# Performance work log

Measured on AMD Instinct MI355X. Metric: run time of the kernel, lower is better.

The kernel has to match this reference:

```python
import jax, jax.numpy as jnp
import numpy as np


def setup_inputs() -> dict:
    key = jax.random.key(0)
    k1, k2 = jax.random.split(key, 2)
    B, C, N, O, K = 4, 3, 8192, 64, 20
    x = jax.random.normal(k1, (B, C, N), dtype=jnp.float32)          # point cloud [B,3,N]
    W = jax.random.normal(k2, (O, 2 * C), dtype=jnp.float32) * 0.1   # 1x1 conv weight on 2C edge features
    b = jnp.zeros((O,), dtype=jnp.float32)
    return {"x": x, "W": W, "b": b, "k": K}


def _knn_idx(x, k):
    # x: [B, C, N]. Same math as torch knn(): pd = -||xi||^2 + 2 xi.xj - ||xj||^2,
    # topk of pd (largest) == k nearest neighbors.
    inner = -2.0 * jnp.einsum('bcn,bcm->bnm', x, x)      # [B,N,N]
    xx = jnp.sum(x * x, axis=1)                          # [B,N]
    pd = -xx[:, :, None] - inner - xx[:, None, :]        # [B,N,N] negative sq-dist
    _, idx = jax.lax.top_k(pd, k)                        # [B,N,k]
    return idx


def reference(x, W, b, k):
    # Faithful jax version of knn + get_graph_feature + 1x1 conv + LeakyReLU + max over k
    # (DGCNN EdgeConv layer, the hot path of the encoder).
    B, C, N = x.shape
    idx = _knn_idx(x, k)                                  # [B,N,k]
    xt = jnp.transpose(x, (0, 2, 1))                      # [B,N,C]
    nb = xt[jnp.arange(B)[:, None, None], idx]            # gather neighbors [B,N,k,C]
    cen = xt[:, :, None, :]                               # [B,N,1,C]
    feat = jnp.concatenate(
        [nb - cen, jnp.broadcast_to(cen, (B, N, k, C))], axis=-1)  # [B,N,k,2C]
    h = jnp.einsum('bnkc,oc->bonk', feat, W) + b[None, :, None, None]  # [B,O,N,k]
    h = jax.nn.leaky_relu(h, negative_slope=0.2)
    return jnp.max(h, axis=-1)                            # [B,O,N]
```

## Files before the change

kernel.cpp:

```cpp
#include <hip/hip_runtime.h>
#include <cstdint>

#pragma clang fp contract(off)

#define N_PTS 8192
#define B_SZ  4
#define K_NN  20
#define O_CH  64
#define QW    64
#define NWAVE 8
#define WARM  64
#define CAPQ  56
#define SPADQ 57
#define NCH   5

typedef unsigned long long u64k;

__device__ __forceinline__ float pd_np(float qx, float qy, float qz, float xxn,
                                       float cx, float cy, float cz, float xm) {
  float p0 = qx * cx;
  float p1 = qy * cy;
  float p2 = qz * cz;
  float dot = (p0 + p1) + p2;
  float t = __builtin_fmaf(dot, 2.0f, -xxn);
  return t - xm;
}

__device__ __forceinline__ void insert20(float (&arr)[K_NN], float v) {
  float c = v;
#pragma unroll
  for (int u = K_NN - 1; u >= 0; --u) {
    float hi = fmaxf(arr[u], c);
    c = fminf(arr[u], c);
    arr[u] = hi;
  }
}

__device__ __forceinline__ void insK(u64k (&a)[K_NN], u64k k) {
  u64k c = k;
#pragma unroll
  for (int u = K_NN - 1; u >= 0; --u) {
    bool g = a[u] > c;
    u64k hi = g ? a[u] : c;
    u64k lo = g ? c : a[u];
    a[u] = hi;
    c = lo;
  }
}

__device__ __forceinline__ unsigned sortable32(float pd) {
  unsigned s = __float_as_uint(pd);
  return s ^ ((unsigned)((int)s >> 31) | 0x80000000u);
}

__device__ __forceinline__ u64k packKey(float pd, int j) {
  return ((u64k)sortable32(pd) << 13) | (unsigned)(8191 - j);
}

__device__ __forceinline__ float keyPd(u64k k) {
  unsigned sp = (unsigned)(k >> 13);
  unsigned s = (sp & 0x80000000u) ? (sp & 0x7FFFFFFFu) : ~sp;
  return __uint_as_float(s);
}

__global__ __launch_bounds__(256, 2)
void pack_kernel(const float* __restrict__ x, float4* __restrict__ P) {
  int idx = blockIdx.x * 256 + threadIdx.x;
  if (idx >= B_SZ * N_PTS) return;
  int b = idx >> 13;
  int n = idx & (N_PTS - 1);
  const float* xb = x + (size_t)b * 3 * N_PTS;
  float x0 = xb[n];
  float x1 = xb[n + N_PTS];
  float x2 = xb[n + 2 * N_PTS];
  float xxv = (x0 * x0 + x1 * x1) + x2 * x2;
  P[idx] = make_float4(x0, x1, x2, xxv);
}

__global__ __launch_bounds__(512, 4)
void knn_edgeconv_kernel(const float4* __restrict__ P,
                         const float* __restrict__ W,
                         const float* __restrict__ bias,
                         float* __restrict__ out) {
  __shared__ u64k  smem[5376];
  __shared__ float tau_l[QW];
  __shared__ int   cnt_l[QW];
  __shared__ int   list_l[QW][21];

  const int t  = threadIdx.x;
  const int ql = t & 63;
  const int s  = t >> 6;
  const int wb = blockIdx.x;
  const int b  = wb >> 7;
  const int n0 = (wb & 127) << 6;
  const int q  = n0 + ql;

  const float4* __restrict__ Pb = P + (size_t)b * N_PTS;
  const float4* __restrict__ Pq = Pb + n0;

  const float4 qc = Pb[q];
  const float qx = qc.x, qy = qc.y, qz = qc.z, xxn = qc.w;

  const int sw  = __builtin_amdgcn_readfirstlane(s);
  const int myq = (sw << 3) + ql;

  float arrv[K_NN];
#pragma unroll
  for (int i = 0; i < K_NN; ++i) arrv[i] = -__builtin_inff();
  {
    const int jb = sw * WARM;
    for (int jj = 0; jj < WARM; ++jj) {
      float4 cd = Pb[jb + jj];
      float pdv = pd_np(qx, qy, qz, xxn, cd.x, cd.y, cd.z, cd.w);
      if (pdv > arrv[0]) insert20(arrv, pdv);
    }
    float* WV = (float*)smem;
#pragma unroll
    for (int i = 0; i < K_NN; ++i) WV[t * 21 + i] = arrv[i];
  }
  __syncthreads();

  u64k karr[K_NN];
#pragma unroll
  for (int i = 0; i < K_NN; ++i) karr[i] = 0ULL;
  if (ql < 8) {
    const float* WV = (const float*)smem;
    float m[K_NN];
#pragma unroll
    for (int i = 0; i < K_NN; ++i) m[i] = -__builtin_inff();
    for (int p = 0; p < NWAVE; ++p) {
      const float* pv = WV + ((p << 6) + myq) * 21;
      for (int i = 0; i < K_NN; ++i) {
        float v = pv[i];
        if (v > m[0]) insert20(m, v);
      }
    }
    tau_l[myq] = m[0];
    cnt_l[myq] = 0;
  }
  __syncthreads();

  const int CB[NCH + 1] = {0, 512, 1024, 2048, 4096, 8192};
  u64k* stk = smem;

  for (int c = 0; c < NCH; ++c) {
    {
      const int csz  = CB[c + 1] - CB[c];
      const int nbat = csz >> 9;
      const int jb   = CB[c] + sw * (csz >> 3);
      const int tau_own = __float_as_int(tau_l[ql]);
      for (int bt = 0; bt < nbat; ++bt) {
        const int j = jb + (bt << 6) + ql;
        const float4 cd = Pb[j];
        const float cx = cd.x, cy = cd.y, cz = cd.z, cw = cd.w;
#pragma unroll 4
        for (int qi = 0; qi < QW; ++qi) {
          const float4 qv = Pq[qi];
          const float stau = __int_as_float(__builtin_amdgcn_readlane(tau_own, qi));
          float pdv = pd_np(qv.x, qv.y, qv.z, qv.w, cx, cy, cz, cw);
          if (pdv >= stau) {
            int slot = atomicAdd(&cnt_l[qi], 1);
            if (slot < CAPQ)
              stk[qi * SPADQ + slot] =
                  ((u64k)__float_as_uint(pdv) << 32) | (unsigned)j;
          }
        }
      }
    }
    __syncthreads();

    if (ql < 8) {
      const float tauc = tau_l[myq];
      const int pc = cnt_l[myq];
      if (pc <= CAPQ) {
        for (int i = 0; i < pc; ++i) {
          u64k e = stk[myq * SPADQ + i];
          float pdv = __uint_as_float((unsigned)(e >> 32));
          int jv = (int)(e & 0xFFFFFFFFu);
          u64k k = packKey(pdv, jv);
          if (k > karr[0]) insK(karr, k);
        }
      } else {
        float4 mq = Pq[myq];
        for (int j = CB[c]; j < CB[c + 1]; ++j) {
          float4 cd = Pb[j];
          float pdv = pd_np(mq.x, mq.y, mq.z, mq.w, cd.x, cd.y, cd.z, cd.w);
          if (pdv >= tauc) {
            u64k k = packKey(pdv, j);
            if (k > karr[0]) insK(karr, k);
          }
        }
      }
      cnt_l[myq] = 0;
      float t20 = keyPd(karr[0]);
      tau_l[myq] = fmaxf(tauc, t20);
    }
    __syncthreads();
  }

  if (ql < 8) {
#pragma unroll
    for (int i = 0; i < K_NN; ++i)
      list_l[myq][i] = 8191 - (int)(karr[i] & 8191ULL);
  }
  __syncthreads();

  float acc[8];
#pragma unroll
  for (int oi = 0; oi < 8; ++oi) acc[oi] = -__builtin_inff();
  const int o0 = s * 8;
  const float* __restrict__ Wp = W + o0 * 6;

  for (int nb = 0; nb < K_NN; ++nb) {
    int m = list_l[ql][nb] & (N_PTS - 1);
    float4 cm = Pb[m];
    float dx = cm.x - qx;
    float dy = cm.y - qy;
    float dz = cm.z - qz;
#pragma unroll
    for (int oi = 0; oi < 8; ++oi) {
      float h = __builtin_fmaf(dz, Wp[oi * 6 + 2],
                __builtin_fmaf(dy, Wp[oi * 6 + 1], dx * Wp[oi * 6 + 0]));
      acc[oi] = fmaxf(acc[oi], h);
    }
  }

#pragma unroll
  for (int oi = 0; oi < 8; ++oi) {
    int o = o0 + oi;
    float base = __builtin_fmaf(qz, Wp[oi * 6 + 5],
                 __builtin_fmaf(qy, Wp[oi * 6 + 4], qx * Wp[oi * 6 + 3])) + bias[o];
    float v = acc[oi] + base;
    v = fmaxf(v, 0.2f * v);
    out[((size_t)(b * O_CH + o) << 13) + q] = v;
  }
}

extern "C" void kernel_launch(void* const* d_in, const int* in_sizes, int n_in,
                              void* d_out, int out_size, void* d_ws, size_t ws_size,
                              hipStream_t stream) {
  const float* x    = (const float*)d_in[0];
  const float* W    = (const float*)d_in[1];
  const float* bias = (const float*)d_in[2];
  float4* P  = (float4*)d_ws;
  float* out = (float*)d_out;

  pack_kernel<<<dim3((B_SZ * N_PTS + 255) / 256), dim3(256), 0, stream>>>(x, P);
  knn_edgeconv_kernel<<<dim3(B_SZ * (N_PTS / QW)), dim3(512), 0, stream>>>(P, W, bias, out);
}
```

Measured before the change: 402.0 us.

## Screen kNN candidates with split-bf16 MFMA distance tiles before exact fp32 rescoring

Replaces the scalar fp32 candidate-screening loop with MFMA 16x16x32 bf16 matrix products. Coordinates and squared norms are split into hi/lo bf16 pairs, so each tile yields an approximate inner-product-minus-norm score. Candidates passing a relaxed threshold (tau plus norm minus EPS) are stored as indices only and rescored in exact fp32 during the per-query merge. The five chunks become two passes, and the per-query stack capacity grows. The cost is extra LDS staging and syncs per 512-point chunk, plus a correctness risk if the EPS margin fails to cover bf16 error and true neighbors are dropped.

```diff
diff --git a/kernel.cpp b/kernel.cpp
--- a/kernel.cpp
+++ b/kernel.cpp
@@ -10,11 +10,24 @@
 #define QW    64
 #define NWAVE 8
 #define WARM  64
-#define CAPQ  56
-#define SPADQ 57
-#define NCH   5
+#define CAPQ  120
+#define EPS   0.05f
+#define P1END 2048
+#define CHUNK 512
 
 typedef unsigned long long u64k;
+typedef unsigned short u16;
+typedef __attribute__((ext_vector_type(8))) __bf16 bf16x8;
+typedef __attribute__((ext_vector_type(8))) unsigned short u16x8;
+typedef __attribute__((ext_vector_type(4))) float f32x4;
+
+__device__ __forceinline__ u16 bf16_rn(float v) {
+  unsigned u = __float_as_uint(v);
+  return (u16)((u + 0x7FFFu + ((u >> 16) & 1u)) >> 16);
+}
+__device__ __forceinline__ float bf16_tof(u16 b) {
+  return __uint_as_float(((unsigned)b) << 16);
+}
 
 __device__ __forceinline__ float pd_np(float qx, float qy, float qz, float xxn,
                                        float cx, float cy, float cz, float xm) {
@@ -48,15 +61,13 @@
   }
 }
 
-__device__ __forceinline__ unsigned sortable32(float pd) {
-  unsigned s = __float_as_uint(pd);
+__device__ __forceinline__ unsigned sortable32(float v) {
+  unsigned s = __float_as_uint(v);
   return s ^ ((unsigned)((int)s >> 31) | 0x80000000u);
 }
-
 __device__ __forceinline__ u64k packKey(float pd, int j) {
   return ((u64k)sortable32(pd) << 13) | (unsigned)(8191 - j);
 }
-
 __device__ __forceinline__ float keyPd(u64k k) {
   unsigned sp = (unsigned)(k >> 13);
   unsigned s = (sp & 0x80000000u) ? (sp & 0x7FFFFFFFu) : ~sp;
@@ -64,26 +75,42 @@
 }
 
 __global__ __launch_bounds__(256, 2)
-void pack_kernel(const float* __restrict__ x, float4* __restrict__ P) {
+void prep_kernel(const float* __restrict__ x, float4* __restrict__ P,
+                 u16* __restrict__ Bp) {
   int idx = blockIdx.x * 256 + threadIdx.x;
   if (idx >= B_SZ * N_PTS) return;
-  int b = idx >> 13;
-  int n = idx & (N_PTS - 1);
+  int b = idx >> 13, n = idx & (N_PTS - 1);
   const float* xb = x + (size_t)b * 3 * N_PTS;
-  float x0 = xb[n];
-  float x1 = xb[n + N_PTS];
-  float x2 = xb[n + 2 * N_PTS];
-  float xxv = (x0 * x0 + x1 * x1) + x2 * x2;
-  P[idx] = make_float4(x0, x1, x2, xxv);
+  float c0 = xb[n], c1 = xb[n + N_PTS], c2 = xb[n + 2 * N_PTS];
+  float xx = (c0 * c0 + c1 * c1) + c2 * c2;
+  P[idx] = make_float4(c0, c1, c2, xx);
+  union { u16 r[8]; uint4 v; } u;
+  float cc[3] = {c0, c1, c2};
+#pragma unroll
+  for (int k = 0; k < 3; ++k) {
+    u16 hb = bf16_rn(cc[k]);
+    u.r[k] = hb;
+    u.r[3 + k] = bf16_rn(cc[k] - bf16_tof(hb));
+  }
+  u16 mh = bf16_rn(-xx);
+  u.r[6] = mh;
+  u.r[7] = bf16_rn(-xx - bf16_tof(mh));
+  ((uint4*)Bp)[idx] = u.v;
 }
 
 __global__ __launch_bounds__(512, 4)
 void knn_edgeconv_kernel(const float4* __restrict__ P,
+                         const u16* __restrict__ Bp,
                          const float* __restrict__ W,
                          const float* __restrict__ bias,
                          float* __restrict__ out) {
-  __shared__ u64k  smem[5376];
+  __shared__ __align__(16) char raw[49152];
+  int*  stk  = (int*)raw;
+  u16*  Blds = (u16*)(raw + 30720);
+  u16*  Alds = (u16*)(raw + 47104);
+  float* WV  = (float*)raw;
   __shared__ float tau_l[QW];
+  __shared__ float xq_l[QW];
   __shared__ int   cnt_l[QW];
   __shared__ int   list_l[QW][21];
 
@@ -95,14 +122,12 @@
   const int n0 = (wb & 127) << 6;
   const int q  = n0 + ql;
 
-  const float4* __restrict__ Pb = P + (size_t)b * N_PTS;
-  const float4* __restrict__ Pq = Pb + n0;
+  const float4* __restrict__ Pb  = P + (size_t)b * N_PTS;
+  const u16*    __restrict__ Bpb = Bp + (size_t)b * N_PTS * 8;
 
   const float4 qc = Pb[q];
   const float qx = qc.x, qy = qc.y, qz = qc.z, xxn = qc.w;
-
-  const int sw  = __builtin_amdgcn_readfirstlane(s);
-  const int myq = (sw << 3) + ql;
+  const int sw = __builtin_amdgcn_readfirstlane(s);
 
   float arrv[K_NN];
 #pragma unroll
@@ -114,75 +139,133 @@
       float pdv = pd_np(qx, qy, qz, xxn, cd.x, cd.y, cd.z, cd.w);
       if (pdv > arrv[0]) insert20(arrv, pdv);
     }
-    float* WV = (float*)smem;
 #pragma unroll
     for (int i = 0; i < K_NN; ++i) WV[t * 21 + i] = arrv[i];
   }
   __syncthreads();
 
-  u64k karr[K_NN];
-#pragma unroll
-  for (int i = 0; i < K_NN; ++i) karr[i] = 0ULL;
-  if (ql < 8) {
-    const float* WV = (const float*)smem;
+  if (t < QW) {
     float m[K_NN];
 #pragma unroll
     for (int i = 0; i < K_NN; ++i) m[i] = -__builtin_inff();
     for (int p = 0; p < NWAVE; ++p) {
-      const float* pv = WV + ((p << 6) + myq) * 21;
+      const float* pv = WV + ((p << 6) + t) * 21;
       for (int i = 0; i < K_NN; ++i) {
         float v = pv[i];
         if (v > m[0]) insert20(m, v);
       }
     }
-    tau_l[myq] = m[0];
-    cnt_l[myq] = 0;
+    tau_l[t] = m[0];
+    float4 pc = Pb[n0 + t];
+    xq_l[t] = pc.w;
+    cnt_l[t] = 0;
+    union { u16 r[16]; uint4 v[2]; } ua;
+    float cc[3] = {pc.x, pc.y, pc.z};
+#pragma unroll
+    for (int k = 0; k < 3; ++k) {
+      u16 hb = bf16_rn(cc[k]);
+      float hf = bf16_tof(hb);
+      u16 lb = bf16_rn(cc[k] - hf);
+      u16 h2 = bf16_rn(2.0f * hf);
+      u16 l2 = bf16_rn(2.0f * bf16_tof(lb));
+      ua.r[k] = h2; ua.r[3 + k] = l2; ua.r[6 + k] = h2;
+    }
+    ua.r[9] = 0x3F80; ua.r[10] = 0x3F80;
+    ua.r[11] = 0; ua.r[12] = 0; ua.r[13] = 0; ua.r[14] = 0; ua.r[15] = 0;
+    ((uint4*)(Alds + t * 16))[0] = ua.v[0];
+    ((uint4*)(Alds + t * 16))[1] = ua.v[1];
   }
   __syncthreads();
 
-  const int CB[NCH + 1] = {0, 512, 1024, 2048, 4096, 8192};
-  u64k* stk = smem;
-
-  for (int c = 0; c < NCH; ++c) {
-    {
-      const int csz  = CB[c + 1] - CB[c];
-      const int nbat = csz >> 9;
-      const int jb   = CB[c] + sw * (csz >> 3);
-      const int tau_own = __float_as_int(tau_l[ql]);
-      for (int bt = 0; bt < nbat; ++bt) {
-        const int j = jb + (bt << 6) + ql;
-        const float4 cd = Pb[j];
-        const float cx = cd.x, cy = cd.y, cz = cd.z, cw = cd.w;
+  const int rt   = s & 3;
+  const int kg   = ql >> 4;
+  const int col  = ql & 15;
+  bf16x8 afrag;
+  if (kg < 2) {
+    u16x8 av = *(const u16x8*)(Alds + (rt * 16 + col) * 16 + kg * 8);
+    afrag = __builtin_bit_cast(bf16x8, av);
+  } else {
+    u16x8 z = {0, 0, 0, 0, 0, 0, 0, 0};
+    afrag = __builtin_bit_cast(bf16x8, z);
+  }
+
+  u64k karr[K_NN];
+#pragma unroll
+  for (int i = 0; i < K_NN; ++i) karr[i] = 0ULL;
+
+  for (int ps = 0; ps < 2; ++ps) {
+    const int lo = ps ? P1END : 0;
+    const int hi = ps ? N_PTS : P1END;
+    float tpe[4];
+#pragma unroll
+    for (int i = 0; i < 4; ++i) {
+      int qr = rt * 16 + ((ql >> 4) << 2) + i;
+      tpe[i] = tau_l[qr] + xq_l[qr] - EPS;
+    }
+    for (int cb = lo; cb < hi; cb += CHUNK) {
+      {
+        uint4 sv = ((const uint4*)(Bpb + (size_t)(cb + t) * 8))[0];
+        unsigned u0 = sv.x, u1 = sv.y, u2 = sv.z, u3 = sv.w;
+        uint4 d0, d1;
+        d0.x = u0;
+        d0.y = (u1 & 0xFFFFu) | (u0 << 16);
+        d0.z = (u0 >> 16) | (u1 << 16);
+        d0.w = (u1 >> 16) | (u2 << 16);
+        d1.x = (u2 >> 16) | (u3 << 16);
+        d1.y = (u3 >> 16);
+        d1.z = 0; d1.w = 0;
+        ((uint4*)(Blds + t * 16))[0] = d0;
+        ((uint4*)(Blds + t * 16))[1] = d1;
+      }
+      __syncthreads();
+      const int tbase = (s >> 2) * 16;
 #pragma unroll 4
-        for (int qi = 0; qi < QW; ++qi) {
-          const float4 qv = Pq[qi];
-          const float stau = __int_as_float(__builtin_amdgcn_readlane(tau_own, qi));
-          float pdv = pd_np(qv.x, qv.y, qv.z, qv.w, cx, cy, cz, cw);
-          if (pdv >= stau) {
-            int slot = atomicAdd(&cnt_l[qi], 1);
-            if (slot < CAPQ)
-              stk[qi * SPADQ + slot] =
-                  ((u64k)__float_as_uint(pdv) << 32) | (unsigned)j;
+      for (int tt = 0; tt < 16; ++tt) {
+        const int tile = tbase + tt;
+        bf16x8 bfrag;
+        if (kg < 2) {
+          u16x8 bv = *(const u16x8*)(Blds + (tile * 16 + col) * 16 + kg * 8);
+          bfrag = __builtin_bit_cast(bf16x8, bv);
+        } else {
+          u16x8 z = {0, 0, 0, 0, 0, 0, 0, 0};
+          bfrag = __builtin_bit_cast(bf16x8, z);
+        }
+        f32x4 acc = {0.0f, 0.0f, 0.0f, 0.0f};
+        acc = __builtin_amdgcn_mfma_f32_16x16x32_bf16(afrag, bfrag, acc, 0, 0, 0);
+        bool f0 = acc[0] >= tpe[0], f1 = acc[1] >= tpe[1];
+        bool f2 = acc[2] >= tpe[2], f3 = acc[3] >= tpe[3];
+        if (__ballot(f0 | f1 | f2 | f3)) {
+          const int candj = cb + tile * 16 + col;
+#pragma unroll
+          for (int i = 0; i < 4; ++i) {
+            bool fi = (i == 0) ? f0 : (i == 1) ? f1 : (i == 2) ? f2 : f3;
+            if (fi) {
+              int qr = rt * 16 + ((ql >> 4) << 2) + i;
+              int slot = atomicAdd(&cnt_l[qr], 1);
+              if (slot < CAPQ) stk[qr * CAPQ + slot] = candj;
+            }
           }
         }
       }
-    }
-    __syncthreads();
-
+      __syncthreads();
+    }
     if (ql < 8) {
+      const int myq = sw * 8 + ql;
       const float tauc = tau_l[myq];
       const int pc = cnt_l[myq];
+      float4 mq = Pb[n0 + myq];
       if (pc <= CAPQ) {
         for (int i = 0; i < pc; ++i) {
-          u64k e = stk[myq * SPADQ + i];
-          float pdv = __uint_as_float((unsigned)(e >> 32));
-          int jv = (int)(e & 0xFFFFFFFFu);
-          u64k k = packKey(pdv, jv);
-          if (k > karr[0]) insK(karr, k);
+          int j = stk[myq * CAPQ + i];
+          float4 cd = Pb[j];
+          float pdv = pd_np(mq.x, mq.y, mq.z, mq.w, cd.x, cd.y, cd.z, cd.w);
+          if (pdv >= tauc) {
+            u64k k = packKey(pdv, j);
+            if (k > karr[0]) insK(karr, k);
+          }
         }
       } else {
-        float4 mq = Pq[myq];
-        for (int j = CB[c]; j < CB[c + 1]; ++j) {
+        for (int j = lo; j < hi; ++j) {
           float4 cd = Pb[j];
           float pdv = pd_np(mq.x, mq.y, mq.z, mq.w, cd.x, cd.y, cd.z, cd.w);
           if (pdv >= tauc) {
@@ -199,6 +282,7 @@
   }
 
   if (ql < 8) {
+    const int myq = sw * 8 + ql;
 #pragma unroll
     for (int i = 0; i < K_NN; ++i)
       list_l[myq][i] = 8191 - (int)(karr[i] & 8191ULL);
@@ -242,9 +326,12 @@
   const float* x    = (const float*)d_in[0];
   const float* W    = (const float*)d_in[1];
   const float* bias = (const float*)d_in[2];
-  float4* P  = (float4*)d_ws;
+  char* ws = (char*)d_ws;
+  float4* P = (float4*)ws;
+  u16*    Bp = (u16*)(ws + 512 * 1024);
   float* out = (float*)d_out;
 
-  pack_kernel<<<dim3((B_SZ * N_PTS + 255) / 256), dim3(256), 0, stream>>>(x, P);
-  knn_edgeconv_kernel<<<dim3(B_SZ * (N_PTS / QW)), dim3(512), 0, stream>>>(P, W, bias, out);
-}
+  prep_kernel<<<dim3((B_SZ * N_PTS + 255) / 256), dim3(256), 0, stream>>>(x, P, Bp);
+  knn_edgeconv_kernel<<<dim3(B_SZ * (N_PTS / QW)), dim3(512), 0, stream>>>(
+      P, Bp, W, bias, out);
+}
```

Result: slower. 1.599 ms (+297.7%).
